# Optimization experiments

Hardware: AMD Instinct MI355X
Metric: run time of the kernel (lower is better)

## Reference

```python
import jax, jax.numpy as jnp
import numpy as np

B, K, T = 64, 256, 64      # batch, num_tokens (feature dim of e / Dense units), word tokens
DF, N = 768, 1024          # image feature channels, spatial regions


def setup_inputs() -> dict:
    key = jax.random.key(0)
    k1, k2, k3 = jax.random.split(key, 3)
    e = jax.random.normal(k1, (B, K, T), dtype=jnp.float32)
    f = jax.random.normal(k2, (B, DF, N), dtype=jnp.float32)
    # Dense(units=K) kernel/bias (Glorot-ish scale)
    W = jax.random.normal(k3, (DF, K), dtype=jnp.float32) / np.sqrt(DF)
    b = jnp.zeros((K,), dtype=jnp.float32)
    gamma = jnp.float32(5.0)  # DAMSM smoothing factor gamma1
    return {"e": e, "f": f, "gamma": gamma, "W": W, "b": b}


def reference(e, f, gamma, W, b):
    # v = transpose(Dense(transpose(f))): project image features Df -> K. [B,K,N]
    v = jnp.einsum('bdn,dk->bkn', f, W) + b[None, :, None]
    # attention scores between word tokens and regions: [B,T,N]
    s = jnp.einsum('bkt,bkn->btn', e, v)
    # gamma-scaled softmax over regions (axis=2)
    alpha = jax.nn.softmax(gamma * s, axis=2)
    # region-context vectors per token: [B,K,T]
    c = jnp.einsum('bkn,btn->bkt', v, alpha)
    # per-token feature norms (reduce over feature axis 1): [B,T]
    lc = jnp.sqrt(jnp.sum(c * c, axis=1))
    le = jnp.sqrt(jnp.sum(e * e, axis=1))
    # token-token cosine similarity: contract feature axis, normalize by outer(lc, le)
    cos = jnp.einsum('bki,bkj->bij', c, e) / (lc[:, :, None] * le[:, None, :])
    return cos
```

## Files before the change

### kernel.cpp

```cpp
#include <hip/hip_runtime.h>

#define B_  64
#define K_  256
#define T_  64
#define DF_ 768
#define N_  1024

typedef __attribute__((ext_vector_type(8))) short bf16x8;
typedef __attribute__((ext_vector_type(4))) float f32x4;

__device__ __forceinline__ unsigned short bf_rne(float x) {
    unsigned u = __float_as_uint(x);
    unsigned r = u + 0x7fffu + ((u >> 16) & 1u);
    return (unsigned short)(r >> 16);
}

__global__ __launch_bounds__(256) void prep_w(const float* __restrict__ W,
                                              unsigned short* __restrict__ W_hi,
                                              unsigned short* __restrict__ W_lo,
                                              unsigned short* __restrict__ WT_hi) {
    int d = blockIdx.x, k = threadIdx.x;
    float w = W[d * K_ + k];
    unsigned u = __float_as_uint(w);
    unsigned short hs = (unsigned short)(u >> 16);
    float hi = __uint_as_float(u & 0xffff0000u);
    W_hi[d * K_ + k]  = hs;
    W_lo[d * K_ + k]  = bf_rne(w - hi);
    WT_hi[k * DF_ + d] = hs;
}

__global__ __launch_bounds__(256) void prep_e(const float* __restrict__ e,
                                              unsigned short* __restrict__ eT_hi,
                                              unsigned short* __restrict__ eT_lo) {
    int b = blockIdx.x;
    int t = threadIdx.x & 63, kq = threadIdx.x >> 6;
    const float* eb = e + (size_t)b * K_ * T_;
    unsigned short* eh = eT_hi + (size_t)b * T_ * K_;
    unsigned short* el = eT_lo + (size_t)b * T_ * K_;
    for (int i = 0; i < 64; i++) {
        int k = kq * 64 + i;
        float x = eb[k * T_ + t];
        unsigned u = __float_as_uint(x);
        unsigned short hs = (unsigned short)(u >> 16);
        float hi = __uint_as_float(u & 0xffff0000u);
        eh[t * K_ + k] = hs;
        el[t * K_ + k] = bf_rne(x - hi);
    }
}

__global__ __launch_bounds__(256, 1) void gemm_g(const unsigned short* __restrict__ eT_hi,
                                                 const unsigned short* __restrict__ eT_lo,
                                                 const unsigned short* __restrict__ W_hi,
                                                 const unsigned short* __restrict__ W_lo,
                                                 unsigned short* __restrict__ gT_hi,
                                                 unsigned short* __restrict__ gT_lo) {
    __shared__ unsigned short LeH[64 * 40], LeL[64 * 40];
    __shared__ unsigned short LwH[128 * 40], LwL[128 * 40];
    const int dblk = blockIdx.x * 128;
    const int b = blockIdx.y;
    const int tid = threadIdx.x;
    const int lane = tid & 63, w = tid >> 6, q = lane >> 4, l16 = lane & 15;

    const unsigned short* eh = eT_hi + (size_t)b * T_ * K_;
    const unsigned short* el = eT_lo + (size_t)b * T_ * K_;

    f32x4 acc[4][2];
#pragma unroll
    for (int i = 0; i < 4; i++)
#pragma unroll
        for (int j = 0; j < 2; j++) acc[i][j] = (f32x4)(0.f);

    for (int k0 = 0; k0 < K_; k0 += 32) {
        {
            int tr = tid >> 2, c8 = (tid & 3) * 8;
            *(uint4*)&LeH[tr * 40 + c8] = *(const uint4*)&eh[tr * K_ + k0 + c8];
            *(uint4*)&LeL[tr * 40 + c8] = *(const uint4*)&el[tr * K_ + k0 + c8];
#pragma unroll
            for (int l = 0; l < 2; l++) {
                int idx = tid + l * 256;
                int r = idx >> 2, cc = (idx & 3) * 8;
                *(uint4*)&LwH[r * 40 + cc] = *(const uint4*)&W_hi[(size_t)(dblk + r) * K_ + k0 + cc];
                *(uint4*)&LwL[r * 40 + cc] = *(const uint4*)&W_lo[(size_t)(dblk + r) * K_ + k0 + cc];
            }
        }
        __syncthreads();
        bf16x8 aH[4], aL[4], bH[2], bL[2];
#pragma unroll
        for (int mt = 0; mt < 4; mt++) {
            aH[mt] = *(const bf16x8*)&LeH[(mt * 16 + l16) * 40 + q * 8];
            aL[mt] = *(const bf16x8*)&LeL[(mt * 16 + l16) * 40 + q * 8];
        }
#pragma unroll
        for (int nt = 0; nt < 2; nt++) {
            int dl = w * 32 + nt * 16 + l16;
            bH[nt] = *(const bf16x8*)&LwH[dl * 40 + q * 8];
            bL[nt] = *(const bf16x8*)&LwL[dl * 40 + q * 8];
        }
#pragma unroll
        for (int mt = 0; mt < 4; mt++)
#pragma unroll
            for (int nt = 0; nt < 2; nt++) {
                acc[mt][nt] = __builtin_amdgcn_mfma_f32_16x16x32_bf16(aH[mt], bH[nt], acc[mt][nt], 0, 0, 0);
                acc[mt][nt] = __builtin_amdgcn_mfma_f32_16x16x32_bf16(aH[mt], bL[nt], acc[mt][nt], 0, 0, 0);
                acc[mt][nt] = __builtin_amdgcn_mfma_f32_16x16x32_bf16(aL[mt], bH[nt], acc[mt][nt], 0, 0, 0);
            }
        __syncthreads();
    }

    unsigned short* gh = gT_hi + (size_t)b * T_ * DF_;
    unsigned short* gl = gT_lo + (size_t)b * T_ * DF_;
#pragma unroll
    for (int mt = 0; mt < 4; mt++)
#pragma unroll
        for (int nt = 0; nt < 2; nt++)
#pragma unroll
            for (int r = 0; r < 4; r++) {
                float x = acc[mt][nt][r];
                int t = mt * 16 + q * 4 + r;
                int d = dblk + w * 32 + nt * 16 + l16;
                unsigned u = __float_as_uint(x);
                unsigned short hs = (unsigned short)(u >> 16);
                float hi = __uint_as_float(u & 0xffff0000u);
                gh[t * DF_ + d] = hs;
                gl[t * DF_ + d] = bf_rne(x - hi);
            }
}

__global__ __launch_bounds__(256, 1) void gemm_s(const unsigned short* __restrict__ gT_hi,
                                                 const unsigned short* __restrict__ gT_lo,
                                                 const float* __restrict__ f,
                                                 float* __restrict__ s) {
    __shared__ unsigned short LgH[64 * 40], LgL[64 * 40];
    __shared__ unsigned LfH[256 * 20], LfL[256 * 20];

    const int flat = blockIdx.x;
    const int b    = (flat & 7) * 8 + (flat >> 5);
    const int nblk = ((flat >> 3) & 3) * 256;
    const int tid = threadIdx.x;
    const int lane = tid & 63, w = tid >> 6, q = lane >> 4, l16 = lane & 15;

    const unsigned short* gh = gT_hi + (size_t)b * T_ * DF_;
    const unsigned short* gl = gT_lo + (size_t)b * T_ * DF_;

    f32x4 acc[4][4];
#pragma unroll
    for (int i = 0; i < 4; i++)
#pragma unroll
        for (int j = 0; j < 4; j++) acc[i][j] = (f32x4)(0.f);

    const int dp = tid >> 4;
    const int nb = (tid & 15) * 4;

    for (int d0 = 0; d0 < DF_; d0 += 32) {
        {
            int tr = tid >> 2, c8 = (tid & 3) * 8;
            *(uint4*)&LgH[tr * 40 + c8] = *(const uint4*)&gh[tr * DF_ + d0 + c8];
            *(uint4*)&LgL[tr * 40 + c8] = *(const uint4*)&gl[tr * DF_ + d0 + c8];
            const float* fb = f + ((size_t)b * DF_ + d0 + dp * 2) * N_ + nblk;
#pragma unroll
            for (int it = 0; it < 4; it++) {
                int n = nb + it * 64;
                float4 x = *(const float4*)&fb[n];
                float4 y = *(const float4*)&fb[N_ + n];
                const float xs[4] = {x.x, x.y, x.z, x.w};
                const float ys[4] = {y.x, y.y, y.z, y.w};
#pragma unroll
                for (int j = 0; j < 4; j++) {
                    unsigned bx = __float_as_uint(xs[j]);
                    unsigned by = __float_as_uint(ys[j]);
                    unsigned hp = (bx >> 16) | (by & 0xffff0000u);
                    float lx = xs[j] - __uint_as_float(bx & 0xffff0000u);
                    float ly = ys[j] - __uint_as_float(by & 0xffff0000u);
                    unsigned lp = (__float_as_uint(lx) >> 16) | (__float_as_uint(ly) & 0xffff0000u);
                    LfH[(n + j) * 20 + dp] = hp;
                    LfL[(n + j) * 20 + dp] = lp;
                }
            }
        }
        __syncthreads();
        bf16x8 aH[4], aL[4], bH[4], bL[4];
#pragma unroll
        for (int mt = 0; mt < 4; mt++) {
            aH[mt] = *(const bf16x8*)&LgH[(mt * 16 + l16) * 40 + q * 8];
            aL[mt] = *(const bf16x8*)&LgL[(mt * 16 + l16) * 40 + q * 8];
        }
#pragma unroll
        for (int nt = 0; nt < 4; nt++) {
            int nl = w * 64 + nt * 16 + l16;
            bH[nt] = *(const bf16x8*)&((const unsigned short*)LfH)[nl * 40 + q * 8];
            bL[nt] = *(const bf16x8*)&((const unsigned short*)LfL)[nl * 40 + q * 8];
        }
#pragma unroll
        for (int mt = 0; mt < 4; mt++)
#pragma unroll
            for (int nt = 0; nt < 4; nt++) {
                acc[mt][nt] = __builtin_amdgcn_mfma_f32_16x16x32_bf16(aH[mt], bH[nt], acc[mt][nt], 0, 0, 0);
                acc[mt][nt] = __builtin_amdgcn_mfma_f32_16x16x32_bf16(aH[mt], bL[nt], acc[mt][nt], 0, 0, 0);
                acc[mt][nt] = __builtin_amdgcn_mfma_f32_16x16x32_bf16(aL[mt], bH[nt], acc[mt][nt], 0, 0, 0);
            }
        __syncthreads();
    }

    float* sb = s + (size_t)b * T_ * N_;
#pragma unroll
    for (int mt = 0; mt < 4; mt++)
#pragma unroll
        for (int nt = 0; nt < 4; nt++)
#pragma unroll
            for (int r = 0; r < 4; r++) {
                int t = mt * 16 + q * 4 + r;
                int n = nblk + w * 64 + nt * 16 + l16;
                sb[(size_t)t * N_ + n] = acc[mt][nt][r];
            }
}

__global__ __launch_bounds__(256) void softmax_k(const float* __restrict__ s,
                                                 unsigned short* __restrict__ alpha,
                                                 const float* __restrict__ gptr) {
    const float g = gptr[0];
    const float* row = s + (size_t)blockIdx.x * N_;
    unsigned short* arow = alpha + (size_t)blockIdx.x * N_;
    const int t = threadIdx.x;

    float4 x = *(const float4*)(row + t * 4);
    x.x *= g; x.y *= g; x.z *= g; x.w *= g;

    float m = fmaxf(fmaxf(x.x, x.y), fmaxf(x.z, x.w));
#pragma unroll
    for (int off = 32; off > 0; off >>= 1) m = fmaxf(m, __shfl_xor(m, off, 64));
    __shared__ float sm[4], ss[4];
    int wave = t >> 6;
    if ((t & 63) == 0) sm[wave] = m;
    __syncthreads();
    m = fmaxf(fmaxf(sm[0], sm[1]), fmaxf(sm[2], sm[3]));

    float e0 = __expf(x.x - m), e1 = __expf(x.y - m);
    float e2 = __expf(x.z - m), e3 = __expf(x.w - m);
    float sum = e0 + e1 + e2 + e3;
#pragma unroll
    for (int off = 32; off > 0; off >>= 1) sum += __shfl_xor(sum, off, 64);
    if ((t & 63) == 0) ss[wave] = sum;
    __syncthreads();
    sum = ss[0] + ss[1] + ss[2] + ss[3];
    float inv = 1.f / sum;
    unsigned p0 = (unsigned)bf_rne(e0 * inv) | ((unsigned)bf_rne(e1 * inv) << 16);
    unsigned p1 = (unsigned)bf_rne(e2 * inv) | ((unsigned)bf_rne(e3 * inv) << 16);
    uint2 o; o.x = p0; o.y = p1;
    *(uint2*)&arow[t * 4] = o;
}

__global__ __launch_bounds__(256, 1) void gemm_h(const float* __restrict__ f,
                                                 const unsigned short* __restrict__ alpha,
                                                 unsigned short* __restrict__ hT) {
    __shared__ unsigned short Lf[128 * 72];
    __shared__ unsigned short La[64 * 72];
    const int dblk = blockIdx.x * 128;
    const int b = blockIdx.y;
    const int tid = threadIdx.x;
    const int lane = tid & 63, w = tid >> 6, q = lane >> 4, l16 = lane & 15;

    const float* fb = f + (size_t)b * DF_ * N_;
    const unsigned short* ab = alpha + (size_t)b * T_ * N_;

    f32x4 acc[2][4];
#pragma unroll
    for (int i = 0; i < 2; i++)
#pragma unroll
        for (int j = 0; j < 4; j++) acc[i][j] = (f32x4)(0.f);

    for (int n0 = 0; n0 < N_; n0 += 64) {
#pragma unroll
        for (int l = 0; l < 8; l++) {
            int idx = tid + l * 256;
            int r = idx >> 4, c4 = idx & 15;
            float4 x = *(const float4*)&fb[(size_t)(dblk + r) * N_ + n0 + c4 * 4];
            unsigned p0 = (unsigned)bf_rne(x.x) | ((unsigned)bf_rne(x.y) << 16);
            unsigned p1 = (unsigned)bf_rne(x.z) | ((unsigned)bf_rne(x.w) << 16);
            uint2 o; o.x = p0; o.y = p1;
            *(uint2*)&Lf[r * 72 + c4 * 4] = o;
        }
#pragma unroll
        for (int l = 0; l < 2; l++) {
            int idx = tid + l * 256;
            int r = idx >> 3, c8 = (idx & 7) * 8;
            *(uint4*)&La[r * 72 + c8] = *(const uint4*)&ab[(size_t)r * N_ + n0 + c8];
        }
        __syncthreads();
        bf16x8 af[2][2], bb[4][2];
#pragma unroll
        for (int mt = 0; mt < 2; mt++)
#pragma unroll
            for (int kk = 0; kk < 2; kk++)
                af[mt][kk] = *(const bf16x8*)&Lf[(w * 32 + mt * 16 + l16) * 72 + kk * 32 + q * 8];
#pragma unroll
        for (int nt = 0; nt < 4; nt++)
#pragma unroll
            for (int kk = 0; kk < 2; kk++)
                bb[nt][kk] = *(const bf16x8*)&La[(nt * 16 + l16) * 72 + kk * 32 + q * 8];
#pragma unroll
        for (int mt = 0; mt < 2; mt++)
#pragma unroll
            for (int nt = 0; nt < 4; nt++)
#pragma unroll
                for (int kk = 0; kk < 2; kk++)
                    acc[mt][nt] = __builtin_amdgcn_mfma_f32_16x16x32_bf16(af[mt][kk], bb[nt][kk], acc[mt][nt], 0, 0, 0);
        __syncthreads();
    }

    unsigned short* hb = hT + (size_t)b * T_ * DF_;
#pragma unroll
    for (int mt = 0; mt < 2; mt++)
#pragma unroll
        for (int nt = 0; nt < 4; nt++)
#pragma unroll
            for (int r = 0; r < 4; r++) {
                int d = dblk + w * 32 + mt * 16 + q * 4 + r;
                int t = nt * 16 + l16;
                hb[(size_t)t * DF_ + d] = bf_rne(acc[mt][nt][r]);
            }
}

__global__ __launch_bounds__(256, 1) void gemm_c(const unsigned short* __restrict__ WT_hi,
                                                 const unsigned short* __restrict__ hT,
                                                 const float* __restrict__ bias,
                                                 float* __restrict__ c) {
    __shared__ unsigned short LW[128 * 72];
    __shared__ unsigned short Lh[64 * 72];
    const int kblk = blockIdx.x * 128;
    const int b = blockIdx.y;
    const int tid = threadIdx.x;
    const int lane = tid & 63, w = tid >> 6, q = lane >> 4, l16 = lane & 15;

    const unsigned short* hb = hT + (size_t)b * T_ * DF_;

    f32x4 acc[2][4];
#pragma unroll
    for (int i = 0; i < 2; i++)
#pragma unroll
        for (int j = 0; j < 4; j++) acc[i][j] = (f32x4)(0.f);

    for (int d0 = 0; d0 < DF_; d0 += 64) {
#pragma unroll
        for (int l = 0; l < 4; l++) {
            int idx = tid + l * 256;
            int r = idx >> 3, c8 = (idx & 7) * 8;
            *(uint4*)&LW[r * 72 + c8] = *(const uint4*)&WT_hi[(size_t)(kblk + r) * DF_ + d0 + c8];
        }
#pragma unroll
        for (int l = 0; l < 2; l++) {
            int idx = tid + l * 256;
            int r = idx >> 3, c8 = (idx & 7) * 8;
            *(uint4*)&Lh[r * 72 + c8] = *(const uint4*)&hb[(size_t)r * DF_ + d0 + c8];
        }
        __syncthreads();
        bf16x8 aw[2][2], bh[4][2];
#pragma unroll
        for (int mt = 0; mt < 2; mt++)
#pragma unroll
            for (int kk = 0; kk < 2; kk++)
                aw[mt][kk] = *(const bf16x8*)&LW[(w * 32 + mt * 16 + l16) * 72 + kk * 32 + q * 8];
#pragma unroll
        for (int nt = 0; nt < 4; nt++)
#pragma unroll
            for (int kk = 0; kk < 2; kk++)
                bh[nt][kk] = *(const bf16x8*)&Lh[(nt * 16 + l16) * 72 + kk * 32 + q * 8];
#pragma unroll
        for (int mt = 0; mt < 2; mt++)
#pragma unroll
            for (int nt = 0; nt < 4; nt++)
#pragma unroll
                for (int kk = 0; kk < 2; kk++)
                    acc[mt][nt] = __builtin_amdgcn_mfma_f32_16x16x32_bf16(aw[mt][kk], bh[nt][kk], acc[mt][nt], 0, 0, 0);
        __syncthreads();
    }

    float* cb = c + (size_t)b * K_ * T_;
#pragma unroll
    for (int mt = 0; mt < 2; mt++)
#pragma unroll
        for (int nt = 0; nt < 4; nt++)
#pragma unroll
            for (int r = 0; r < 4; r++) {
                int k = kblk + w * 32 + mt * 16 + q * 4 + r;
                int t = nt * 16 + l16;
                cb[(size_t)k * T_ + t] = acc[mt][nt][r] + bias[k];
            }
}

__global__ __launch_bounds__(64) void cos_k(const float* __restrict__ c,
                                            const float* __restrict__ e,
                                            float* __restrict__ out) {
    const int i = blockIdx.x;
    const int b = blockIdx.y;
    const int j = threadIdx.x;
    const float* cb = c + (size_t)b * K_ * T_;
    const float* eb = e + (size_t)b * K_ * T_;

    float dot = 0.f, se = 0.f, sc = 0.f;
#pragma unroll 8
    for (int k = 0; k < K_; k++) {
        float cv = cb[(size_t)k * T_ + i];
        float ev = eb[(size_t)k * T_ + j];
        dot += cv * ev;
        se  += ev * ev;
        sc  += cv * cv;
    }
    out[((size_t)b * T_ + i) * T_ + j] = dot * rsqrtf(sc * se);
}

extern "C" void kernel_launch(void* const* d_in, const int* in_sizes, int n_in,
                              void* d_out, int out_size, void* d_ws, size_t ws_size,
                              hipStream_t stream) {
    const float* e     = (const float*)d_in[0];
    const float* f     = (const float*)d_in[1];
    const float* gamma = (const float*)d_in[2];
    const float* W     = (const float*)d_in[3];
    const float* bias  = (const float*)d_in[4];
    float* out = (float*)d_out;

    char* p = (char*)d_ws;
    unsigned short* W_hi  = (unsigned short*)p; p += (size_t)DF_ * K_ * 2;
    unsigned short* W_lo  = (unsigned short*)p; p += (size_t)DF_ * K_ * 2;
    unsigned short* WT_hi = (unsigned short*)p; p += (size_t)DF_ * K_ * 2;
    unsigned short* eT_hi = (unsigned short*)p; p += (size_t)B_ * T_ * K_ * 2;
    unsigned short* eT_lo = (unsigned short*)p; p += (size_t)B_ * T_ * K_ * 2;
    unsigned short* gT_hi = (unsigned short*)p; p += (size_t)B_ * T_ * DF_ * 2;
    unsigned short* gT_lo = (unsigned short*)p; p += (size_t)B_ * T_ * DF_ * 2;
    float*          s     = (float*)p;          p += (size_t)B_ * T_ * N_ * 4;
    unsigned short* alpha = (unsigned short*)p; p += (size_t)B_ * T_ * N_ * 2;
    unsigned short* hT    = (unsigned short*)p; p += (size_t)B_ * T_ * DF_ * 2;
    float*          c     = (float*)p;          p += (size_t)B_ * K_ * T_ * 4;

    prep_w  <<<dim3(DF_),          256, 0, stream>>>(W, W_hi, W_lo, WT_hi);
    prep_e  <<<dim3(B_),           256, 0, stream>>>(e, eT_hi, eT_lo);
    gemm_g  <<<dim3(DF_ / 128, B_),256, 0, stream>>>(eT_hi, eT_lo, W_hi, W_lo, gT_hi, gT_lo);
    gemm_s  <<<dim3(256),          256, 0, stream>>>(gT_hi, gT_lo, f, s);
    softmax_k<<<dim3(B_ * T_),     256, 0, stream>>>(s, alpha, gamma);
    gemm_h  <<<dim3(DF_ / 128, B_),256, 0, stream>>>(f, alpha, hT);
    gemm_c  <<<dim3(K_ / 128, B_), 256, 0, stream>>>(WT_hi, hT, bias, c);
    cos_k   <<<dim3(T_, B_),       64,  0, stream>>>(c, e, out);
}
```

Before: 410.5 us.

## Halve GEMM tile sizes for more blocks, merge prep kernels, widen cos blocks

Halves the output tile of the gemm_g, gemm_s, gemm_h and gemm_c kernels and raises launch bounds to two blocks per CU. This doubles grid sizes so more waves fill the 256 CUs on MI355X. It also merges prep_w and prep_e into one launch, spreads the e transposition over more blocks, rotates the LDS write order in gemm_s to reduce bank conflicts, and packs four cos rows per 256-thread block. Smaller tiles lower per-block data reuse and increase total global and LDS traffic.

```diff
diff --git a/kernel.cpp b/kernel.cpp
--- a/kernel.cpp
+++ b/kernel.cpp
@@ -15,48 +15,52 @@
     return (unsigned short)(r >> 16);
 }
 
-__global__ __launch_bounds__(256) void prep_w(const float* __restrict__ W,
-                                              unsigned short* __restrict__ W_hi,
-                                              unsigned short* __restrict__ W_lo,
-                                              unsigned short* __restrict__ WT_hi) {
-    int d = blockIdx.x, k = threadIdx.x;
-    float w = W[d * K_ + k];
-    unsigned u = __float_as_uint(w);
-    unsigned short hs = (unsigned short)(u >> 16);
-    float hi = __uint_as_float(u & 0xffff0000u);
-    W_hi[d * K_ + k]  = hs;
-    W_lo[d * K_ + k]  = bf_rne(w - hi);
-    WT_hi[k * DF_ + d] = hs;
-}
-
-__global__ __launch_bounds__(256) void prep_e(const float* __restrict__ e,
-                                              unsigned short* __restrict__ eT_hi,
-                                              unsigned short* __restrict__ eT_lo) {
-    int b = blockIdx.x;
-    int t = threadIdx.x & 63, kq = threadIdx.x >> 6;
-    const float* eb = e + (size_t)b * K_ * T_;
-    unsigned short* eh = eT_hi + (size_t)b * T_ * K_;
-    unsigned short* el = eT_lo + (size_t)b * T_ * K_;
-    for (int i = 0; i < 64; i++) {
-        int k = kq * 64 + i;
-        float x = eb[k * T_ + t];
-        unsigned u = __float_as_uint(x);
+__global__ __launch_bounds__(256) void prep_we(const float* __restrict__ W,
+                                               const float* __restrict__ e,
+                                               unsigned short* __restrict__ W_hi,
+                                               unsigned short* __restrict__ W_lo,
+                                               unsigned short* __restrict__ WT_hi,
+                                               unsigned short* __restrict__ eT_hi,
+                                               unsigned short* __restrict__ eT_lo) {
+    int blk = blockIdx.x;
+    if (blk < DF_) {
+        int d = blk, k = threadIdx.x;
+        float w = W[d * K_ + k];
+        unsigned u = __float_as_uint(w);
         unsigned short hs = (unsigned short)(u >> 16);
         float hi = __uint_as_float(u & 0xffff0000u);
-        eh[t * K_ + k] = hs;
-        el[t * K_ + k] = bf_rne(x - hi);
-    }
-}
-
-__global__ __launch_bounds__(256, 1) void gemm_g(const unsigned short* __restrict__ eT_hi,
+        W_hi[d * K_ + k]   = hs;
+        W_lo[d * K_ + k]   = bf_rne(w - hi);
+        WT_hi[k * DF_ + d] = hs;
+    } else {
+        int q = blk - DF_;
+        int b = q >> 2, kq = q & 3;
+        int t = threadIdx.x & 63, ko = threadIdx.x >> 6;
+        const float* eb = e + (size_t)b * K_ * T_;
+        unsigned short* eh = eT_hi + (size_t)b * T_ * K_;
+        unsigned short* el = eT_lo + (size_t)b * T_ * K_;
+#pragma unroll
+        for (int i = 0; i < 16; i++) {
+            int k = kq * 64 + ko * 16 + i;
+            float x = eb[k * T_ + t];
+            unsigned u = __float_as_uint(x);
+            unsigned short hs = (unsigned short)(u >> 16);
+            float hi = __uint_as_float(u & 0xffff0000u);
+            eh[t * K_ + k] = hs;
+            el[t * K_ + k] = bf_rne(x - hi);
+        }
+    }
+}
+
+__global__ __launch_bounds__(256, 2) void gemm_g(const unsigned short* __restrict__ eT_hi,
                                                  const unsigned short* __restrict__ eT_lo,
                                                  const unsigned short* __restrict__ W_hi,
                                                  const unsigned short* __restrict__ W_lo,
                                                  unsigned short* __restrict__ gT_hi,
                                                  unsigned short* __restrict__ gT_lo) {
     __shared__ unsigned short LeH[64 * 40], LeL[64 * 40];
-    __shared__ unsigned short LwH[128 * 40], LwL[128 * 40];
-    const int dblk = blockIdx.x * 128;
+    __shared__ unsigned short LwH[64 * 40], LwL[64 * 40];
+    const int dblk = blockIdx.x * 64;
     const int b = blockIdx.y;
     const int tid = threadIdx.x;
     const int lane = tid & 63, w = tid >> 6, q = lane >> 4, l16 = lane & 15;
@@ -64,37 +68,115 @@
     const unsigned short* eh = eT_hi + (size_t)b * T_ * K_;
     const unsigned short* el = eT_lo + (size_t)b * T_ * K_;
 
-    f32x4 acc[4][2];
-#pragma unroll
-    for (int i = 0; i < 4; i++)
-#pragma unroll
-        for (int j = 0; j < 2; j++) acc[i][j] = (f32x4)(0.f);
-
+    f32x4 acc[4];
+#pragma unroll
+    for (int i = 0; i < 4; i++) acc[i] = (f32x4)(0.f);
+
+    const int tr = tid >> 2, c8 = (tid & 3) * 8;
     for (int k0 = 0; k0 < K_; k0 += 32) {
-        {
-            int tr = tid >> 2, c8 = (tid & 3) * 8;
-            *(uint4*)&LeH[tr * 40 + c8] = *(const uint4*)&eh[tr * K_ + k0 + c8];
-            *(uint4*)&LeL[tr * 40 + c8] = *(const uint4*)&el[tr * K_ + k0 + c8];
-#pragma unroll
-            for (int l = 0; l < 2; l++) {
-                int idx = tid + l * 256;
-                int r = idx >> 2, cc = (idx & 3) * 8;
-                *(uint4*)&LwH[r * 40 + cc] = *(const uint4*)&W_hi[(size_t)(dblk + r) * K_ + k0 + cc];
-                *(uint4*)&LwL[r * 40 + cc] = *(const uint4*)&W_lo[(size_t)(dblk + r) * K_ + k0 + cc];
-            }
-        }
-        __syncthreads();
-        bf16x8 aH[4], aL[4], bH[2], bL[2];
+        *(uint4*)&LeH[tr * 40 + c8] = *(const uint4*)&eh[tr * K_ + k0 + c8];
+        *(uint4*)&LeL[tr * 40 + c8] = *(const uint4*)&el[tr * K_ + k0 + c8];
+        *(uint4*)&LwH[tr * 40 + c8] = *(const uint4*)&W_hi[(size_t)(dblk + tr) * K_ + k0 + c8];
+        *(uint4*)&LwL[tr * 40 + c8] = *(const uint4*)&W_lo[(size_t)(dblk + tr) * K_ + k0 + c8];
+        __syncthreads();
+        bf16x8 aH[4], aL[4], bH, bL;
 #pragma unroll
         for (int mt = 0; mt < 4; mt++) {
             aH[mt] = *(const bf16x8*)&LeH[(mt * 16 + l16) * 40 + q * 8];
             aL[mt] = *(const bf16x8*)&LeL[(mt * 16 + l16) * 40 + q * 8];
         }
+        int dl = w * 16 + l16;
+        bH = *(const bf16x8*)&LwH[dl * 40 + q * 8];
+        bL = *(const bf16x8*)&LwL[dl * 40 + q * 8];
+#pragma unroll
+        for (int mt = 0; mt < 4; mt++) {
+            acc[mt] = __builtin_amdgcn_mfma_f32_16x16x32_bf16(aH[mt], bH, acc[mt], 0, 0, 0);
+            acc[mt] = __builtin_amdgcn_mfma_f32_16x16x32_bf16(aH[mt], bL, acc[mt], 0, 0, 0);
+            acc[mt] = __builtin_amdgcn_mfma_f32_16x16x32_bf16(aL[mt], bH, acc[mt], 0, 0, 0);
+        }
+        __syncthreads();
+    }
+
+    unsigned short* gh = gT_hi + (size_t)b * T_ * DF_;
+    unsigned short* gl = gT_lo + (size_t)b * T_ * DF_;
+#pragma unroll
+    for (int mt = 0; mt < 4; mt++)
+#pragma unroll
+        for (int r = 0; r < 4; r++) {
+            float x = acc[mt][r];
+            int t = mt * 16 + q * 4 + r;
+            int d = dblk + w * 16 + l16;
+            unsigned u = __float_as_uint(x);
+            unsigned short hs = (unsigned short)(u >> 16);
+            float hi = __uint_as_float(u & 0xffff0000u);
+            gh[t * DF_ + d] = hs;
+            gl[t * DF_ + d] = bf_rne(x - hi);
+        }
+}
+
+__global__ __launch_bounds__(256, 2) void gemm_s(const unsigned short* __restrict__ gT_hi,
+                                                 const unsigned short* __restrict__ gT_lo,
+                                                 const float* __restrict__ f,
+                                                 float* __restrict__ s) {
+    __shared__ unsigned short LgH[64 * 40], LgL[64 * 40];
+    __shared__ unsigned LfH[128 * 20], LfL[128 * 20];
+
+    const int flat = blockIdx.x;
+    const int b    = (flat & 7) * 8 + ((flat >> 3) & 7);
+    const int nblk = (flat >> 6) * 128;
+    const int tid = threadIdx.x;
+    const int lane = tid & 63, w = tid >> 6, q = lane >> 4, l16 = lane & 15;
+
+    const unsigned short* gh = gT_hi + (size_t)b * T_ * DF_;
+    const unsigned short* gl = gT_lo + (size_t)b * T_ * DF_;
+
+    f32x4 acc[4][2];
+#pragma unroll
+    for (int i = 0; i < 4; i++)
+#pragma unroll
+        for (int j = 0; j < 2; j++) acc[i][j] = (f32x4)(0.f);
+
+    const int dp  = tid >> 4;
+    const int nb  = (tid & 15) * 8;
+    const int rot = tid & 7;
+    const int tr = tid >> 2, c8 = (tid & 3) * 8;
+
+    for (int d0 = 0; d0 < DF_; d0 += 32) {
+        *(uint4*)&LgH[tr * 40 + c8] = *(const uint4*)&gh[tr * DF_ + d0 + c8];
+        *(uint4*)&LgL[tr * 40 + c8] = *(const uint4*)&gl[tr * DF_ + d0 + c8];
+        {
+            const float* fp = f + ((size_t)b * DF_ + d0 + dp * 2) * N_ + nblk + nb;
+            float4 x0 = *(const float4*)&fp[0];
+            float4 x1 = *(const float4*)&fp[4];
+            float4 y0 = *(const float4*)&fp[N_ + 0];
+            float4 y1 = *(const float4*)&fp[N_ + 4];
+            const float xs[8] = {x0.x, x0.y, x0.z, x0.w, x1.x, x1.y, x1.z, x1.w};
+            const float ys[8] = {y0.x, y0.y, y0.z, y0.w, y1.x, y1.y, y1.z, y1.w};
+#pragma unroll
+            for (int jj = 0; jj < 8; jj++) {
+                int j = (jj + rot) & 7;
+                unsigned bx = __float_as_uint(xs[j]);
+                unsigned by = __float_as_uint(ys[j]);
+                unsigned hp = (bx >> 16) | (by & 0xffff0000u);
+                float lx = xs[j] - __uint_as_float(bx & 0xffff0000u);
+                float ly = ys[j] - __uint_as_float(by & 0xffff0000u);
+                unsigned lp = (__float_as_uint(lx) >> 16) | (__float_as_uint(ly) & 0xffff0000u);
+                LfH[(nb + j) * 20 + dp] = hp;
+                LfL[(nb + j) * 20 + dp] = lp;
+            }
+        }
+        __syncthreads();
+        bf16x8 aH[4], aL[4], bH[2], bL[2];
+#pragma unroll
+        for (int mt = 0; mt < 4; mt++) {
+            aH[mt] = *(const bf16x8*)&LgH[(mt * 16 + l16) * 40 + q * 8];
+            aL[mt] = *(const bf16x8*)&LgL[(mt * 16 + l16) * 40 + q * 8];
+        }
 #pragma unroll
         for (int nt = 0; nt < 2; nt++) {
-            int dl = w * 32 + nt * 16 + l16;
-            bH[nt] = *(const bf16x8*)&LwH[dl * 40 + q * 8];
-            bL[nt] = *(const bf16x8*)&LwL[dl * 40 + q * 8];
+            int nl = w * 32 + nt * 16 + l16;
+            bH[nt] = *(const bf16x8*)&((const unsigned short*)LfH)[nl * 40 + q * 8];
+            bL[nt] = *(const bf16x8*)&((const unsigned short*)LfL)[nl * 40 + q * 8];
         }
 #pragma unroll
         for (int mt = 0; mt < 4; mt++)
@@ -107,109 +189,15 @@
         __syncthreads();
     }
 
-    unsigned short* gh = gT_hi + (size_t)b * T_ * DF_;
-    unsigned short* gl = gT_lo + (size_t)b * T_ * DF_;
+    float* sb = s + (size_t)b * T_ * N_;
 #pragma unroll
     for (int mt = 0; mt < 4; mt++)
 #pragma unroll
         for (int nt = 0; nt < 2; nt++)
-#pragma unroll
-            for (int r = 0; r < 4; r++) {
-                float x = acc[mt][nt][r];
-                int t = mt * 16 + q * 4 + r;
-                int d = dblk + w * 32 + nt * 16 + l16;
-                unsigned u = __float_as_uint(x);
-                unsigned short hs = (unsigned short)(u >> 16);
-                float hi = __uint_as_float(u & 0xffff0000u);
-                gh[t * DF_ + d] = hs;
-                gl[t * DF_ + d] = bf_rne(x - hi);
-            }
-}
-
-__global__ __launch_bounds__(256, 1) void gemm_s(const unsigned short* __restrict__ gT_hi,
-                                                 const unsigned short* __restrict__ gT_lo,
-                                                 const float* __restrict__ f,
-                                                 float* __restrict__ s) {
-    __shared__ unsigned short LgH[64 * 40], LgL[64 * 40];
-    __shared__ unsigned LfH[256 * 20], LfL[256 * 20];
-
-    const int flat = blockIdx.x;
-    const int b    = (flat & 7) * 8 + (flat >> 5);
-    const int nblk = ((flat >> 3) & 3) * 256;
-    const int tid = threadIdx.x;
-    const int lane = tid & 63, w = tid >> 6, q = lane >> 4, l16 = lane & 15;
-
-    const unsigned short* gh = gT_hi + (size_t)b * T_ * DF_;
-    const unsigned short* gl = gT_lo + (size_t)b * T_ * DF_;
-
-    f32x4 acc[4][4];
-#pragma unroll
-    for (int i = 0; i < 4; i++)
-#pragma unroll
-        for (int j = 0; j < 4; j++) acc[i][j] = (f32x4)(0.f);
-
-    const int dp = tid >> 4;
-    const int nb = (tid & 15) * 4;
-
-    for (int d0 = 0; d0 < DF_; d0 += 32) {
-        {
-            int tr = tid >> 2, c8 = (tid & 3) * 8;
-            *(uint4*)&LgH[tr * 40 + c8] = *(const uint4*)&gh[tr * DF_ + d0 + c8];
-            *(uint4*)&LgL[tr * 40 + c8] = *(const uint4*)&gl[tr * DF_ + d0 + c8];
-            const float* fb = f + ((size_t)b * DF_ + d0 + dp * 2) * N_ + nblk;
-#pragma unroll
-            for (int it = 0; it < 4; it++) {
-                int n = nb + it * 64;
-                float4 x = *(const float4*)&fb[n];
-                float4 y = *(const float4*)&fb[N_ + n];
-                const float xs[4] = {x.x, x.y, x.z, x.w};
-                const float ys[4] = {y.x, y.y, y.z, y.w};
-#pragma unroll
-                for (int j = 0; j < 4; j++) {
-                    unsigned bx = __float_as_uint(xs[j]);
-                    unsigned by = __float_as_uint(ys[j]);
-                    unsigned hp = (bx >> 16) | (by & 0xffff0000u);
-                    float lx = xs[j] - __uint_as_float(bx & 0xffff0000u);
-                    float ly = ys[j] - __uint_as_float(by & 0xffff0000u);
-                    unsigned lp = (__float_as_uint(lx) >> 16) | (__float_as_uint(ly) & 0xffff0000u);
-                    LfH[(n + j) * 20 + dp] = hp;
-                    LfL[(n + j) * 20 + dp] = lp;
-                }
-            }
-        }
-        __syncthreads();
-        bf16x8 aH[4], aL[4], bH[4], bL[4];
-#pragma unroll
-        for (int mt = 0; mt < 4; mt++) {
-            aH[mt] = *(const bf16x8*)&LgH[(mt * 16 + l16) * 40 + q * 8];
-            aL[mt] = *(const bf16x8*)&LgL[(mt * 16 + l16) * 40 + q * 8];
-        }
-#pragma unroll
-        for (int nt = 0; nt < 4; nt++) {
-            int nl = w * 64 + nt * 16 + l16;
-            bH[nt] = *(const bf16x8*)&((const unsigned short*)LfH)[nl * 40 + q * 8];
-            bL[nt] = *(const bf16x8*)&((const unsigned short*)LfL)[nl * 40 + q * 8];
-        }
-#pragma unroll
-        for (int mt = 0; mt < 4; mt++)
-#pragma unroll
-            for (int nt = 0; nt < 4; nt++) {
-                acc[mt][nt] = __builtin_amdgcn_mfma_f32_16x16x32_bf16(aH[mt], bH[nt], acc[mt][nt], 0, 0, 0);
-                acc[mt][nt] = __builtin_amdgcn_mfma_f32_16x16x32_bf16(aH[mt], bL[nt], acc[mt][nt], 0, 0, 0);
-                acc[mt][nt] = __builtin_amdgcn_mfma_f32_16x16x32_bf16(aL[mt], bH[nt], acc[mt][nt], 0, 0, 0);
-            }
-        __syncthreads();
-    }
-
-    float* sb = s + (size_t)b * T_ * N_;
-#pragma unroll
-    for (int mt = 0; mt < 4; mt++)
-#pragma unroll
-        for (int nt = 0; nt < 4; nt++)
 #pragma unroll
             for (int r = 0; r < 4; r++) {
                 int t = mt * 16 + q * 4 + r;
-                int n = nblk + w * 64 + nt * 16 + l16;
+                int n = nblk + w * 32 + nt * 16 + l16;
                 sb[(size_t)t * N_ + n] = acc[mt][nt][r];
             }
 }
@@ -249,12 +237,12 @@
     *(uint2*)&arow[t * 4] = o;
 }
 
-__global__ __launch_bounds__(256, 1) void gemm_h(const float* __restrict__ f,
+__global__ __launch_bounds__(256, 2) void gemm_h(const float* __restrict__ f,
                                                  const unsigned short* __restrict__ alpha,
                                                  unsigned short* __restrict__ hT) {
-    __shared__ unsigned short Lf[128 * 72];
+    __shared__ unsigned short Lf[64 * 72];
     __shared__ unsigned short La[64 * 72];
-    const int dblk = blockIdx.x * 128;
+    const int dblk = blockIdx.x * 64;
     const int b = blockIdx.y;
     const int tid = threadIdx.x;
     const int lane = tid & 63, w = tid >> 6, q = lane >> 4, l16 = lane & 15;
@@ -262,137 +250,117 @@
     const float* fb = f + (size_t)b * DF_ * N_;
     const unsigned short* ab = alpha + (size_t)b * T_ * N_;
 
-    f32x4 acc[2][4];
-#pragma unroll
-    for (int i = 0; i < 2; i++)
-#pragma unroll
-        for (int j = 0; j < 4; j++) acc[i][j] = (f32x4)(0.f);
-
+    f32x4 acc[4];
+#pragma unroll
+    for (int i = 0; i < 4; i++) acc[i] = (f32x4)(0.f);
+
+    const int fr_ = tid >> 2, fc = tid & 3;
     for (int n0 = 0; n0 < N_; n0 += 64) {
-#pragma unroll
-        for (int l = 0; l < 8; l++) {
-            int idx = tid + l * 256;
-            int r = idx >> 4, c4 = idx & 15;
-            float4 x = *(const float4*)&fb[(size_t)(dblk + r) * N_ + n0 + c4 * 4];
+        const float* frp = fb + (size_t)(dblk + fr_) * N_ + n0 + fc * 16;
+#pragma unroll
+        for (int i = 0; i < 4; i++) {
+            float4 x = *(const float4*)&frp[i * 4];
             unsigned p0 = (unsigned)bf_rne(x.x) | ((unsigned)bf_rne(x.y) << 16);
             unsigned p1 = (unsigned)bf_rne(x.z) | ((unsigned)bf_rne(x.w) << 16);
             uint2 o; o.x = p0; o.y = p1;
-            *(uint2*)&Lf[r * 72 + c4 * 4] = o;
+            *(uint2*)&Lf[fr_ * 72 + fc * 16 + i * 4] = o;
         }
 #pragma unroll
         for (int l = 0; l < 2; l++) {
-            int idx = tid + l * 256;
+            int idx = tid * 2 + l;
             int r = idx >> 3, c8 = (idx & 7) * 8;
             *(uint4*)&La[r * 72 + c8] = *(const uint4*)&ab[(size_t)r * N_ + n0 + c8];
         }
         __syncthreads();
-        bf16x8 af[2][2], bb[4][2];
-#pragma unroll
-        for (int mt = 0; mt < 2; mt++)
-#pragma unroll
-            for (int kk = 0; kk < 2; kk++)
-                af[mt][kk] = *(const bf16x8*)&Lf[(w * 32 + mt * 16 + l16) * 72 + kk * 32 + q * 8];
+        bf16x8 af[2], bb[4][2];
+#pragma unroll
+        for (int kk = 0; kk < 2; kk++)
+            af[kk] = *(const bf16x8*)&Lf[(w * 16 + l16) * 72 + kk * 32 + q * 8];
 #pragma unroll
         for (int nt = 0; nt < 4; nt++)
 #pragma unroll
             for (int kk = 0; kk < 2; kk++)
                 bb[nt][kk] = *(const bf16x8*)&La[(nt * 16 + l16) * 72 + kk * 32 + q * 8];
 #pragma unroll
-        for (int mt = 0; mt < 2; mt++)
-#pragma unroll
-            for (int nt = 0; nt < 4; nt++)
-#pragma unroll
-                for (int kk = 0; kk < 2; kk++)
-                    acc[mt][nt] = __builtin_amdgcn_mfma_f32_16x16x32_bf16(af[mt][kk], bb[nt][kk], acc[mt][nt], 0, 0, 0);
+        for (int nt = 0; nt < 4; nt++)
+#pragma unroll
+            for (int kk = 0; kk < 2; kk++)
+                acc[nt] = __builtin_amdgcn_mfma_f32_16x16x32_bf16(af[kk], bb[nt][kk], acc[nt], 0, 0, 0);
         __syncthreads();
     }
 
     unsigned short* hb = hT + (size_t)b * T_ * DF_;
 #pragma unroll
-    for (int mt = 0; mt < 2; mt++)
-#pragma unroll
-        for (int nt = 0; nt < 4; nt++)
-#pragma unroll
-            for (int r = 0; r < 4; r++) {
-                int d = dblk + w * 32 + mt * 16 + q * 4 + r;
-                int t = nt * 16 + l16;
-                hb[(size_t)t * DF_ + d] = bf_rne(acc[mt][nt][r]);
-            }
-}
-
-__global__ __launch_bounds__(256, 1) void gemm_c(const unsigned short* __restrict__ WT_hi,
+    for (int nt = 0; nt < 4; nt++)
+#pragma unroll
+        for (int r = 0; r < 4; r++) {
+            int d = dblk + w * 16 + q * 4 + r;
+            int t = nt * 16 + l16;
+            hb[(size_t)t * DF_ + d] = bf_rne(acc[nt][r]);
+        }
+}
+
+__global__ __launch_bounds__(256, 2) void gemm_c(const unsigned short* __restrict__ WT_hi,
                                                  const unsigned short* __restrict__ hT,
                                                  const float* __restrict__ bias,
                                                  float* __restrict__ c) {
-    __shared__ unsigned short LW[128 * 72];
+    __shared__ unsigned short LW[64 * 72];
     __shared__ unsigned short Lh[64 * 72];
-    const int kblk = blockIdx.x * 128;
+    const int kblk = blockIdx.x * 64;
     const int b = blockIdx.y;
     const int tid = threadIdx.x;
     const int lane = tid & 63, w = tid >> 6, q = lane >> 4, l16 = lane & 15;
 
     const unsigned short* hb = hT + (size_t)b * T_ * DF_;
 
-    f32x4 acc[2][4];
-#pragma unroll
-    for (int i = 0; i < 2; i++)
-#pragma unroll
-        for (int j = 0; j < 4; j++) acc[i][j] = (f32x4)(0.f);
+    f32x4 acc[4];
+#pragma unroll
+    for (int i = 0; i < 4; i++) acc[i] = (f32x4)(0.f);
 
     for (int d0 = 0; d0 < DF_; d0 += 64) {
 #pragma unroll
-        for (int l = 0; l < 4; l++) {
-            int idx = tid + l * 256;
+        for (int l = 0; l < 2; l++) {
+            int idx = tid * 2 + l;
             int r = idx >> 3, c8 = (idx & 7) * 8;
             *(uint4*)&LW[r * 72 + c8] = *(const uint4*)&WT_hi[(size_t)(kblk + r) * DF_ + d0 + c8];
-        }
-#pragma unroll
-        for (int l = 0; l < 2; l++) {
-            int idx = tid + l * 256;
-            int r = idx >> 3, c8 = (idx & 7) * 8;
             *(uint4*)&Lh[r * 72 + c8] = *(const uint4*)&hb[(size_t)r * DF_ + d0 + c8];
         }
         __syncthreads();
-        bf16x8 aw[2][2], bh[4][2];
-#pragma unroll
-        for (int mt = 0; mt < 2; mt++)
-#pragma unroll
-            for (int kk = 0; kk < 2; kk++)
-                aw[mt][kk] = *(const bf16x8*)&LW[(w * 32 + mt * 16 + l16) * 72 + kk * 32 + q * 8];
+        bf16x8 aw[2], bh[4][2];
+#pragma unroll
+        for (int kk = 0; kk < 2; kk++)
+            aw[kk] = *(const bf16x8*)&LW[(w * 16 + l16) * 72 + kk * 32 + q * 8];
 #pragma unroll
         for (int nt = 0; nt < 4; nt++)
 #pragma unroll
             for (int kk = 0; kk < 2; kk++)
                 bh[nt][kk] = *(const bf16x8*)&Lh[(nt * 16 + l16) * 72 + kk * 32 + q * 8];
 #pragma unroll
-        for (int mt = 0; mt < 2; mt++)
-#pragma unroll
-            for (int nt = 0; nt < 4; nt++)
-#pragma unroll
-                for (int kk = 0; kk < 2; kk++)
-                    acc[mt][nt] = __builtin_amdgcn_mfma_f32_16x16x32_bf16(aw[mt][kk], bh[nt][kk], acc[mt][nt], 0, 0, 0);
+        for (int nt = 0; nt < 4; nt++)
+#pragma unroll
+            for (int kk = 0; kk < 2; kk++)
+                acc[nt] = __builtin_amdgcn_mfma_f32_16x16x32_bf16(aw[kk], bh[nt][kk], acc[nt], 0, 0, 0);
         __syncthreads();
     }
 
     float* cb = c + (size_t)b * K_ * T_;
 #pragma unroll
-    for (int mt = 0; mt < 2; mt++)
-#pragma unroll
-        for (int nt = 0; nt < 4; nt++)
-#pragma unroll
-            for (int r = 0; r < 4; r++) {
-                int k = kblk + w * 32 + mt * 16 + q * 4 + r;
-                int t = nt * 16 + l16;
-                cb[(size_t)k * T_ + t] = acc[mt][nt][r] + bias[k];
-            }
-}
-
-__global__ __launch_bounds__(64) void cos_k(const float* __restrict__ c,
-                                            const float* __restrict__ e,
-                                            float* __restrict__ out) {
-    const int i = blockIdx.x;
+    for (int nt = 0; nt < 4; nt++)
+#pragma unroll
+        for (int r = 0; r < 4; r++) {
+            int k = kblk + w * 16 + q * 4 + r;
+            int t = nt * 16 + l16;
+            cb[(size_t)k * T_ + t] = acc[nt][r] + bias[k];
+        }
+}
+
+__global__ __launch_bounds__(256) void cos_k(const float* __restrict__ c,
+                                             const float* __restrict__ e,
+                                             float* __restrict__ out) {
+    const int iq = threadIdx.x >> 6;
+    const int i = blockIdx.x * 4 + iq;
     const int b = blockIdx.y;
-    const int j = threadIdx.x;
+    const int j = threadIdx.x & 63;
     const float* cb = c + (size_t)b * K_ * T_;
     const float* eb = e + (size_t)b * K_ * T_;
 
@@ -431,12 +399,11 @@
     unsigned short* hT    = (unsigned short*)p; p += (size_t)B_ * T_ * DF_ * 2;
     float*          c     = (float*)p;          p += (size_t)B_ * K_ * T_ * 4;
 
-    prep_w  <<<dim3(DF_),          256, 0, stream>>>(W, W_hi, W_lo, WT_hi);
-    prep_e  <<<dim3(B_),           256, 0, stream>>>(e, eT_hi, eT_lo);
-    gemm_g  <<<dim3(DF_ / 128, B_),256, 0, stream>>>(eT_hi, eT_lo, W_hi, W_lo, gT_hi, gT_lo);
-    gemm_s  <<<dim3(256),          256, 0, stream>>>(gT_hi, gT_lo, f, s);
-    softmax_k<<<dim3(B_ * T_),     256, 0, stream>>>(s, alpha, gamma);
-    gemm_h  <<<dim3(DF_ / 128, B_),256, 0, stream>>>(f, alpha, hT);
-    gemm_c  <<<dim3(K_ / 128, B_), 256, 0, stream>>>(WT_hi, hT, bias, c);
-    cos_k   <<<dim3(T_, B_),       64,  0, stream>>>(c, e, out);
-}
+    prep_we <<<dim3(DF_ + 256),     256, 0, stream>>>(W, e, W_hi, W_lo, WT_hi, eT_hi, eT_lo);
+    gemm_g  <<<dim3(DF_ / 64, B_),  256, 0, stream>>>(eT_hi, eT_lo, W_hi, W_lo, gT_hi, gT_lo);
+    gemm_s  <<<dim3(512),           256, 0, stream>>>(gT_hi, gT_lo, f, s);
+    softmax_k<<<dim3(B_ * T_),      256, 0, stream>>>(s, alpha, gamma);
+    gemm_h  <<<dim3(DF_ / 64, B_),  256, 0, stream>>>(f, alpha, hT);
+    gemm_c  <<<dim3(K_ / 64, B_),   256, 0, stream>>>(WT_hi, hT, bias, c);
+    cos_k   <<<dim3(T_ / 4, B_),    256, 0, stream>>>(c, e, out);
+}
```

Result: faster. 381.0 us (-7.2%).
